# Kernel optimization log

Measured on AMD Instinct MI355X. Metric: run time of the kernel, lower is better.

## Reference

```python
import jax, jax.numpy as jnp
import numpy as np


def _cdist(a, b):
    # Euclidean pairwise distances, [N, M]
    d2 = (jnp.sum(a * a, axis=1)[:, None]
          + jnp.sum(b * b, axis=1)[None, :]
          - 2.0 * (a @ b.T))
    return jnp.sqrt(jnp.maximum(d2, 0.0))


def setup_inputs() -> dict:
    key = jax.random.key(0)
    k1, k2 = jax.random.split(key)
    N, M, D = 12288, 12288, 3
    true_pos = jax.random.normal(k1, (N, D), dtype=jnp.float32)
    pred_pos = jax.random.normal(k2, (M, D), dtype=jnp.float32)
    return {"true_pos": true_pos, "pred_pos": pred_pos}


def reference(true_pos, pred_pos):
    dists = _cdist(true_pos.astype(jnp.float32), pred_pos.astype(jnp.float32))
    mins = jnp.min(dists, axis=1)        # per true point -> nearest pred
    mins_seeds = jnp.min(dists, axis=0)  # per pred point -> nearest true
    loss = jnp.mean(mins)
    loss_seeds = jnp.mean(mins_seeds)
    just_in_case_losses = (loss, loss_seeds)
    # use_loss=True branch
    return (loss + loss_seeds, mins_seeds, just_in_case_losses)
```

## Files before the change

kernel.cpp:

```cpp
#include <hip/hip_runtime.h>
#include <hip/hip_bf16.h>
#include <cfloat>

#define BLOCK 256
#define RPT 8
#define SLICES 64

static __device__ __forceinline__ unsigned f2key(float f) {
    unsigned b = __float_as_uint(f);
    return (b & 0x80000000u) ? ~b : (b ^ 0x80000000u);
}
static __device__ __forceinline__ float key2f(unsigned k) {
    unsigned b = (k & 0x80000000u) ? (k ^ 0x80000000u) : ~k;
    return __uint_as_float(b);
}

__global__ __launch_bounds__(BLOCK) void pairmin_kernel(
    const float* __restrict__ A, const float* __restrict__ B,
    unsigned* __restrict__ min_a, unsigned* __restrict__ min_b,
    int n, int m, int colsPerSlice)
{
    const float* X; const float* Y;
    unsigned* outmin; int nx_, ny_;
    if (blockIdx.z == 0) { X = A; Y = B; outmin = min_a; nx_ = n; ny_ = m; }
    else                 { X = B; Y = A; outmin = min_b; nx_ = m; ny_ = n; }

    const int tid = threadIdx.x;
    const int rowBase = blockIdx.x * (BLOCK * RPT);
    if (rowBase >= nx_) return;

    const int colBeg = blockIdx.y * colsPerSlice;
    if (colBeg >= ny_) return;
    const int colEnd = min(colBeg + colsPerSlice, ny_);

    float nrx[RPT], nry[RPT], nrz[RPT], mn[RPT];
    bool valid[RPT];
#pragma unroll
    for (int k = 0; k < RPT; ++k) {
        int r = rowBase + tid + k * BLOCK;
        valid[k] = (r < nx_);
        int rr = valid[k] ? r : 0;
        nrx[k] = -X[3 * rr + 0];
        nry[k] = -X[3 * rr + 1];
        nrz[k] = -X[3 * rr + 2];
        mn[k] = FLT_MAX;
    }

    __shared__ float4 cols[BLOCK];
    for (int c0 = colBeg; c0 < colEnd; c0 += BLOCK) {
        const int cnt = min(BLOCK, colEnd - c0);
        if (tid < cnt) {
            const int c = c0 + tid;
            const float yx = Y[3 * c + 0];
            const float yy = Y[3 * c + 1];
            const float yz = Y[3 * c + 2];
            const float halfny = 0.5f * fmaf(yx, yx, fmaf(yy, yy, yz * yz));
            cols[tid] = make_float4(yx, yy, yz, halfny);
        }
        __syncthreads();
#pragma unroll 4
        for (int j = 0; j < cnt; ++j) {
            const float4 cc = cols[j];
#pragma unroll
            for (int k = 0; k < RPT; ++k) {
                float s = fmaf(nrx[k], cc.x,
                          fmaf(nry[k], cc.y,
                          fmaf(nrz[k], cc.z, cc.w)));
                mn[k] = fminf(mn[k], s);
            }
        }
        __syncthreads();
    }

#pragma unroll
    for (int k = 0; k < RPT; ++k) {
        if (valid[k])
            atomicMin(&outmin[rowBase + tid + k * BLOCK], f2key(mn[k]));
    }
}

#define FBLOCKS 128
__global__ __launch_bounds__(256) void finalize_kernel(
    const float* __restrict__ A, const float* __restrict__ B,
    const unsigned* __restrict__ min_a, const unsigned* __restrict__ min_b,
    float* __restrict__ hdr, float* __restrict__ out, int n, int m)
{
    const int stride = gridDim.x * 256;
    const int start = blockIdx.x * 256 + threadIdx.x;

    float sa = 0.f, sb = 0.f;
    for (int i = start; i < n; i += stride) {
        const float ax = A[3 * i + 0], ay = A[3 * i + 1], az = A[3 * i + 2];
        const float nrm = fmaf(ax, ax, fmaf(ay, ay, az * az));
        const float s  = key2f(min_a[i]);
        const float d2 = fmaxf(fmaf(2.f, s, nrm), 0.f);
        sa += sqrtf(d2);
    }
    for (int i = start; i < m; i += stride) {
        const float bx = B[3 * i + 0], by = B[3 * i + 1], bz = B[3 * i + 2];
        const float nrm = fmaf(bx, bx, fmaf(by, by, bz * bz));
        const float s  = key2f(min_b[i]);
        const float d2 = fmaxf(fmaf(2.f, s, nrm), 0.f);
        const float v = sqrtf(d2);
        out[1 + i] = v;
        sb += v;
    }

#pragma unroll
    for (int off = 32; off > 0; off >>= 1) {
        sa += __shfl_down(sa, off, 64);
        sb += __shfl_down(sb, off, 64);
    }
    __shared__ float reda[4], redb[4];
    const int wave = threadIdx.x >> 6;
    const int lane = threadIdx.x & 63;
    if (lane == 0) { reda[wave] = sa; redb[wave] = sb; }
    __syncthreads();

    if (threadIdx.x == 0) {
        float ta = reda[0] + reda[1] + reda[2] + reda[3];
        float tb = redb[0] + redb[1] + redb[2] + redb[3];
        atomicAdd(&hdr[0], ta);
        atomicAdd(&hdr[1], tb);
        __threadfence();
        unsigned ticket = atomicAdd((unsigned*)&hdr[2], 1u);
        if (ticket == (unsigned)(gridDim.x - 1)) {
            const float fa = atomicAdd(&hdr[0], 0.f);
            const float fb = atomicAdd(&hdr[1], 0.f);
            const float loss = fa / (float)n;
            const float loss_seeds = fb / (float)m;
            out[0] = loss + loss_seeds;
            out[1 + m] = loss;
            out[2 + m] = loss_seeds;
        }
    }
}

extern "C" void kernel_launch(void* const* d_in, const int* in_sizes, int n_in,
                              void* d_out, int out_size, void* d_ws, size_t ws_size,
                              hipStream_t stream) {
    const int n = in_sizes[0] / 3;
    const int m = in_sizes[1] / 3;
    const float* A = (const float*)d_in[0];
    const float* B = (const float*)d_in[1];
    float* out = (float*)d_out;

    float* hdr = (float*)d_ws;
    unsigned* min_a = (unsigned*)((char*)d_ws + 32);
    unsigned* min_b = min_a + n;

    hipMemsetAsync(d_ws, 0, 32, stream);
    hipMemsetAsync((void*)min_a, 0xFF, (size_t)(n + m) * 4, stream);

    const int maxnm = (n > m) ? n : m;
    const int gx = (maxnm + BLOCK * RPT - 1) / (BLOCK * RPT);
    const int colsPerSlice = (maxnm + SLICES - 1) / SLICES;
    dim3 grid(gx, SLICES, 2);
    pairmin_kernel<<<grid, BLOCK, 0, stream>>>(A, B, min_a, min_b, n, m, colsPerSlice);

    finalize_kernel<<<FBLOCKS, 256, 0, stream>>>(A, B, min_a, min_b, hdr, out, n, m);
}
```

Measured before the change: 90.84 us.

## Use packed FP32 FMA and per-slice partial minima instead of atomics and memsets

New measurement: 91.36 us. No clear change (+0.6%).

```diff
diff --git a/kernel.cpp b/kernel.cpp
--- a/kernel.cpp
+++ b/kernel.cpp
@@ -1,49 +1,46 @@
 #include <hip/hip_runtime.h>
-#include <hip/hip_bf16.h>
 #include <cfloat>
 
 #define BLOCK 256
 #define RPT 8
+#define PAIRS (RPT / 2)
 #define SLICES 64
 
-static __device__ __forceinline__ unsigned f2key(float f) {
-    unsigned b = __float_as_uint(f);
-    return (b & 0x80000000u) ? ~b : (b ^ 0x80000000u);
-}
-static __device__ __forceinline__ float key2f(unsigned k) {
-    unsigned b = (k & 0x80000000u) ? (k ^ 0x80000000u) : ~k;
-    return __uint_as_float(b);
-}
+typedef float v2f __attribute__((ext_vector_type(2)));
 
 __global__ __launch_bounds__(BLOCK) void pairmin_kernel(
     const float* __restrict__ A, const float* __restrict__ B,
-    unsigned* __restrict__ min_a, unsigned* __restrict__ min_b,
-    int n, int m, int colsPerSlice)
+    float* __restrict__ hdr, float* __restrict__ sbuf,
+    int n, int m, int colsPerSlice, int strideRows)
 {
-    const float* X; const float* Y;
-    unsigned* outmin; int nx_, ny_;
-    if (blockIdx.z == 0) { X = A; Y = B; outmin = min_a; nx_ = n; ny_ = m; }
-    else                 { X = B; Y = A; outmin = min_b; nx_ = m; ny_ = n; }
+    if (blockIdx.x == 0 && blockIdx.y == 0 && blockIdx.z == 0 && threadIdx.x < 8)
+        hdr[threadIdx.x] = 0.f;
+
+    const float* X; const float* Y; int nx_, ny_;
+    float* out_slice;
+    if (blockIdx.z == 0) { X = A; Y = B; nx_ = n; ny_ = m; out_slice = sbuf; }
+    else                 { X = B; Y = A; nx_ = m; ny_ = n;
+                           out_slice = sbuf + (size_t)SLICES * strideRows; }
+    out_slice += (size_t)blockIdx.y * strideRows;
 
     const int tid = threadIdx.x;
     const int rowBase = blockIdx.x * (BLOCK * RPT);
     if (rowBase >= nx_) return;
 
     const int colBeg = blockIdx.y * colsPerSlice;
-    if (colBeg >= ny_) return;
     const int colEnd = min(colBeg + colsPerSlice, ny_);
 
-    float nrx[RPT], nry[RPT], nrz[RPT], mn[RPT];
-    bool valid[RPT];
+    v2f nrx[PAIRS], nry[PAIRS], nrz[PAIRS], mn[PAIRS];
 #pragma unroll
-    for (int k = 0; k < RPT; ++k) {
-        int r = rowBase + tid + k * BLOCK;
-        valid[k] = (r < nx_);
-        int rr = valid[k] ? r : 0;
-        nrx[k] = -X[3 * rr + 0];
-        nry[k] = -X[3 * rr + 1];
-        nrz[k] = -X[3 * rr + 2];
-        mn[k] = FLT_MAX;
+    for (int p = 0; p < PAIRS; ++p) {
+        const int r0 = rowBase + tid + (2 * p) * BLOCK;
+        const int r1 = r0 + BLOCK;
+        const int rr0 = (r0 < nx_) ? r0 : 0;
+        const int rr1 = (r1 < nx_) ? r1 : 0;
+        nrx[p] = (v2f){-X[3 * rr0 + 0], -X[3 * rr1 + 0]};
+        nry[p] = (v2f){-X[3 * rr0 + 1], -X[3 * rr1 + 1]};
+        nrz[p] = (v2f){-X[3 * rr0 + 2], -X[3 * rr1 + 2]};
+        mn[p] = (v2f){FLT_MAX, FLT_MAX};
     }
 
     __shared__ float4 cols[BLOCK];
@@ -61,49 +58,53 @@
 #pragma unroll 4
         for (int j = 0; j < cnt; ++j) {
             const float4 cc = cols[j];
+            const v2f cx = cc.x, cy = cc.y, cz = cc.z, cw = cc.w;
 #pragma unroll
-            for (int k = 0; k < RPT; ++k) {
-                float s = fmaf(nrx[k], cc.x,
-                          fmaf(nry[k], cc.y,
-                          fmaf(nrz[k], cc.z, cc.w)));
-                mn[k] = fminf(mn[k], s);
+            for (int p = 0; p < PAIRS; ++p) {
+                v2f s = __builtin_elementwise_fma(nrz[p], cz, cw);
+                s = __builtin_elementwise_fma(nry[p], cy, s);
+                s = __builtin_elementwise_fma(nrx[p], cx, s);
+                mn[p] = __builtin_elementwise_min(mn[p], s);
             }
         }
         __syncthreads();
     }
 
 #pragma unroll
-    for (int k = 0; k < RPT; ++k) {
-        if (valid[k])
-            atomicMin(&outmin[rowBase + tid + k * BLOCK], f2key(mn[k]));
+    for (int p = 0; p < PAIRS; ++p) {
+        const int r0 = rowBase + tid + (2 * p) * BLOCK;
+        const int r1 = r0 + BLOCK;
+        if (r0 < nx_) out_slice[r0] = mn[p].x;
+        if (r1 < nx_) out_slice[r1] = mn[p].y;
     }
 }
 
-#define FBLOCKS 128
 __global__ __launch_bounds__(256) void finalize_kernel(
     const float* __restrict__ A, const float* __restrict__ B,
-    const unsigned* __restrict__ min_a, const unsigned* __restrict__ min_b,
-    float* __restrict__ hdr, float* __restrict__ out, int n, int m)
+    const float* __restrict__ sbuf, float* __restrict__ hdr,
+    float* __restrict__ out, int n, int m, int strideRows)
 {
-    const int stride = gridDim.x * 256;
-    const int start = blockIdx.x * 256 + threadIdx.x;
-
+    const int i = blockIdx.x * 256 + threadIdx.x;
     float sa = 0.f, sb = 0.f;
-    for (int i = start; i < n; i += stride) {
-        const float ax = A[3 * i + 0], ay = A[3 * i + 1], az = A[3 * i + 2];
+    if (i < n) {
+        float s = FLT_MAX;
+        const float* p = sbuf + i;
+#pragma unroll 8
+        for (int k = 0; k < SLICES; ++k) s = fminf(s, p[(size_t)k * strideRows]);
+        const float ax = A[3 * i], ay = A[3 * i + 1], az = A[3 * i + 2];
         const float nrm = fmaf(ax, ax, fmaf(ay, ay, az * az));
-        const float s  = key2f(min_a[i]);
-        const float d2 = fmaxf(fmaf(2.f, s, nrm), 0.f);
-        sa += sqrtf(d2);
+        sa = sqrtf(fmaxf(fmaf(2.f, s, nrm), 0.f));
     }
-    for (int i = start; i < m; i += stride) {
-        const float bx = B[3 * i + 0], by = B[3 * i + 1], bz = B[3 * i + 2];
+    if (i < m) {
+        float s = FLT_MAX;
+        const float* p = sbuf + (size_t)SLICES * strideRows + i;
+#pragma unroll 8
+        for (int k = 0; k < SLICES; ++k) s = fminf(s, p[(size_t)k * strideRows]);
+        const float bx = B[3 * i], by = B[3 * i + 1], bz = B[3 * i + 2];
         const float nrm = fmaf(bx, bx, fmaf(by, by, bz * bz));
-        const float s  = key2f(min_b[i]);
-        const float d2 = fmaxf(fmaf(2.f, s, nrm), 0.f);
-        const float v = sqrtf(d2);
+        const float v = sqrtf(fmaxf(fmaf(2.f, s, nrm), 0.f));
         out[1 + i] = v;
-        sb += v;
+        sb = v;
     }
 
 #pragma unroll
@@ -118,12 +119,12 @@
     __syncthreads();
 
     if (threadIdx.x == 0) {
-        float ta = reda[0] + reda[1] + reda[2] + reda[3];
-        float tb = redb[0] + redb[1] + redb[2] + redb[3];
+        const float ta = reda[0] + reda[1] + reda[2] + reda[3];
+        const float tb = redb[0] + redb[1] + redb[2] + redb[3];
         atomicAdd(&hdr[0], ta);
         atomicAdd(&hdr[1], tb);
         __threadfence();
-        unsigned ticket = atomicAdd((unsigned*)&hdr[2], 1u);
+        const unsigned ticket = atomicAdd((unsigned*)&hdr[2], 1u);
         if (ticket == (unsigned)(gridDim.x - 1)) {
             const float fa = atomicAdd(&hdr[0], 0.f);
             const float fb = atomicAdd(&hdr[1], 0.f);
@@ -146,17 +147,15 @@
     float* out = (float*)d_out;
 
     float* hdr = (float*)d_ws;
-    unsigned* min_a = (unsigned*)((char*)d_ws + 32);
-    unsigned* min_b = min_a + n;
-
-    hipMemsetAsync(d_ws, 0, 32, stream);
-    hipMemsetAsync((void*)min_a, 0xFF, (size_t)(n + m) * 4, stream);
+    float* sbuf = (float*)((char*)d_ws + 64);
 
     const int maxnm = (n > m) ? n : m;
     const int gx = (maxnm + BLOCK * RPT - 1) / (BLOCK * RPT);
     const int colsPerSlice = (maxnm + SLICES - 1) / SLICES;
     dim3 grid(gx, SLICES, 2);
-    pairmin_kernel<<<grid, BLOCK, 0, stream>>>(A, B, min_a, min_b, n, m, colsPerSlice);
+    pairmin_kernel<<<grid, BLOCK, 0, stream>>>(A, B, hdr, sbuf, n, m,
+                                               colsPerSlice, maxnm);
 
-    finalize_kernel<<<FBLOCKS, 256, 0, stream>>>(A, B, min_a, min_b, hdr, out, n, m);
+    const int fb = (maxnm + 255) / 256;
+    finalize_kernel<<<fb, 256, 0, stream>>>(A, B, sbuf, hdr, out, n, m, maxnm);
 }
```

## Compute squared distances with bf16 split-precision MFMA and a single shared pass

Applied to the files above, without the earlier changes.

Measured after the change: 269.8 us. +197.0%, slower.

```diff
diff --git a/kernel.cpp b/kernel.cpp
--- a/kernel.cpp
+++ b/kernel.cpp
@@ -1,10 +1,11 @@
 #include <hip/hip_runtime.h>
-#include <hip/hip_bf16.h>
 #include <cfloat>
 
-#define BLOCK 256
-#define RPT 8
-#define SLICES 64
+typedef __bf16 bf16x8 __attribute__((ext_vector_type(8)));
+typedef unsigned short ushort8 __attribute__((ext_vector_type(8)));
+typedef float f32x16 __attribute__((ext_vector_type(16)));
+
+#define S_SLICES 8
 
 static __device__ __forceinline__ unsigned f2key(float f) {
     unsigned b = __float_as_uint(f);
@@ -14,96 +15,136 @@
     unsigned b = (k & 0x80000000u) ? (k ^ 0x80000000u) : ~k;
     return __uint_as_float(b);
 }
-
-__global__ __launch_bounds__(BLOCK) void pairmin_kernel(
+static __device__ __forceinline__ unsigned short f2bf(float x) {
+    unsigned u = __float_as_uint(x);
+    return (unsigned short)((u + 0x7FFFu + ((u >> 16) & 1u)) >> 16);
+}
+static __device__ __forceinline__ float bfbits2f(unsigned short h) {
+    return __uint_as_float(((unsigned)h) << 16);
+}
+
+__global__ __launch_bounds__(256) void prep_kernel(
     const float* __restrict__ A, const float* __restrict__ B,
-    unsigned* __restrict__ min_a, unsigned* __restrict__ min_b,
-    int n, int m, int colsPerSlice)
+    ushort8* __restrict__ AF, ushort8* __restrict__ BF,
+    unsigned* __restrict__ rowkey, unsigned* __restrict__ colkey,
+    float* __restrict__ hdr, int n, int m, int RT, int CT)
 {
-    const float* X; const float* Y;
-    unsigned* outmin; int nx_, ny_;
-    if (blockIdx.z == 0) { X = A; Y = B; outmin = min_a; nx_ = n; ny_ = m; }
-    else                 { X = B; Y = A; outmin = min_b; nx_ = m; ny_ = n; }
-
-    const int tid = threadIdx.x;
-    const int rowBase = blockIdx.x * (BLOCK * RPT);
-    if (rowBase >= nx_) return;
-
-    const int colBeg = blockIdx.y * colsPerSlice;
-    if (colBeg >= ny_) return;
-    const int colEnd = min(colBeg + colsPerSlice, ny_);
-
-    float nrx[RPT], nry[RPT], nrz[RPT], mn[RPT];
-    bool valid[RPT];
-#pragma unroll
-    for (int k = 0; k < RPT; ++k) {
-        int r = rowBase + tid + k * BLOCK;
-        valid[k] = (r < nx_);
-        int rr = valid[k] ? r : 0;
-        nrx[k] = -X[3 * rr + 0];
-        nry[k] = -X[3 * rr + 1];
-        nrz[k] = -X[3 * rr + 2];
-        mn[k] = FLT_MAX;
-    }
-
-    __shared__ float4 cols[BLOCK];
-    for (int c0 = colBeg; c0 < colEnd; c0 += BLOCK) {
-        const int cnt = min(BLOCK, colEnd - c0);
-        if (tid < cnt) {
-            const int c = c0 + tid;
-            const float yx = Y[3 * c + 0];
-            const float yy = Y[3 * c + 1];
-            const float yz = Y[3 * c + 2];
-            const float halfny = 0.5f * fmaf(yx, yx, fmaf(yy, yy, yz * yz));
-            cols[tid] = make_float4(yx, yy, yz, halfny);
+    const int i = blockIdx.x * 256 + threadIdx.x;
+    if (i < 8) hdr[i] = 0.f;
+    if (i < RT * 32) rowkey[i] = 0xFFFFFFFFu;
+    if (i < CT * 32) colkey[i] = 0xFFFFFFFFu;
+    const unsigned short one = 0x3F80;
+
+    if (i < RT * 32) {
+        float x = 0.f, y = 0.f, z = 0.f, nrm = 1e30f;
+        if (i < n) { x = A[3*i]; y = A[3*i+1]; z = A[3*i+2];
+                     nrm = fmaf(x, x, fmaf(y, y, z * z)); }
+        const unsigned short hx = f2bf(x), hy = f2bf(y), hz = f2bf(z);
+        const unsigned short lx = f2bf(x - bfbits2f(hx)),
+                             ly = f2bf(y - bfbits2f(hy)),
+                             lz = f2bf(z - bfbits2f(hz));
+        const unsigned short nhx = f2bf(-2.f * bfbits2f(hx)),
+                             nhy = f2bf(-2.f * bfbits2f(hy)),
+                             nhz = f2bf(-2.f * bfbits2f(hz));
+        const unsigned short nlx = f2bf(-2.f * bfbits2f(lx)),
+                             nly = f2bf(-2.f * bfbits2f(ly)),
+                             nlz = f2bf(-2.f * bfbits2f(lz));
+        float r = nrm;
+        const unsigned short s1 = f2bf(r); r -= bfbits2f(s1);
+        const unsigned short s2 = f2bf(r); r -= bfbits2f(s2);
+        const unsigned short s3 = f2bf(r);
+        ushort8 q0 = { nhx, nhy, nhz, nhx, nhy, nhz, nlx, nly };
+        ushort8 q1 = { nlz, s1, s2, s3, one, one, one, 0 };
+        const int rt = i >> 5, l5 = i & 31;
+        AF[rt * 64 + l5]      = q0;
+        AF[rt * 64 + 32 + l5] = q1;
+    }
+    if (i < CT * 32) {
+        float x = 0.f, y = 0.f, z = 0.f, nrm = 1e30f;
+        if (i < m) { x = B[3*i]; y = B[3*i+1]; z = B[3*i+2];
+                     nrm = fmaf(x, x, fmaf(y, y, z * z)); }
+        const unsigned short hx = f2bf(x), hy = f2bf(y), hz = f2bf(z);
+        const unsigned short lx = f2bf(x - bfbits2f(hx)),
+                             ly = f2bf(y - bfbits2f(hy)),
+                             lz = f2bf(z - bfbits2f(hz));
+        float r = nrm;
+        const unsigned short s1 = f2bf(r); r -= bfbits2f(s1);
+        const unsigned short s2 = f2bf(r); r -= bfbits2f(s2);
+        const unsigned short s3 = f2bf(r);
+        ushort8 q0 = { hx, hy, hz, lx, ly, lz, hx, hy };
+        ushort8 q1 = { hz, one, one, one, s1, s2, s3, 0 };
+        const int ct = i >> 5, l5 = i & 31;
+        BF[ct * 64 + l5]      = q0;
+        BF[ct * 64 + 32 + l5] = q1;
+    }
+}
+
+__global__ __launch_bounds__(256) void pairmin_kernel(
+    const bf16x8* __restrict__ AF, const bf16x8* __restrict__ BF,
+    unsigned* __restrict__ rowkey, unsigned* __restrict__ colkey,
+    int RT, int CT)
+{
+    const int lane = threadIdx.x & 63;
+    const int wave = threadIdx.x >> 6;
+    const int rt = blockIdx.x * 4 + wave;
+    if (rt >= RT) return;
+
+    const int ctPer = (CT + S_SLICES - 1) / S_SLICES;
+    const int ctBeg = blockIdx.y * ctPer;
+    const int ctEnd = min(ctBeg + ctPer, CT);
+
+    const bf16x8 afrag = AF[rt * 64 + lane];
+
+    float macc[16];
+#pragma unroll
+    for (int r = 0; r < 16; ++r) macc[r] = FLT_MAX;
+
+    for (int ct = ctBeg; ct < ctEnd; ++ct) {
+        const bf16x8 bfrag = BF[ct * 64 + lane];
+        f32x16 C = {};
+        C = __builtin_amdgcn_mfma_f32_32x32x16_bf16(afrag, bfrag, C, 0, 0, 0);
+
+        float cm = fminf(C[0], C[1]);
+#pragma unroll
+        for (int r = 2; r < 16; ++r) cm = fminf(cm, C[r]);
+        cm = fminf(cm, __shfl_xor(cm, 32, 64));
+        atomicMin(&colkey[ct * 32 + (lane & 31)], f2key(cm));
+
+#pragma unroll
+        for (int r = 0; r < 16; ++r) macc[r] = fminf(macc[r], C[r]);
+    }
+
+#pragma unroll
+    for (int r = 0; r < 16; ++r) {
+        float v = macc[r];
+        v = fminf(v, __shfl_xor(v, 1, 64));
+        v = fminf(v, __shfl_xor(v, 2, 64));
+        v = fminf(v, __shfl_xor(v, 4, 64));
+        v = fminf(v, __shfl_xor(v, 8, 64));
+        v = fminf(v, __shfl_xor(v, 16, 64));
+        macc[r] = v;
+    }
+    if ((lane & 31) == 0) {
+        const int q4 = (lane >> 5) * 4;
+#pragma unroll
+        for (int r = 0; r < 16; ++r) {
+            const int row = (r & 3) + 8 * (r >> 2) + q4;
+            atomicMin(&rowkey[rt * 32 + row], f2key(macc[r]));
         }
-        __syncthreads();
-#pragma unroll 4
-        for (int j = 0; j < cnt; ++j) {
-            const float4 cc = cols[j];
-#pragma unroll
-            for (int k = 0; k < RPT; ++k) {
-                float s = fmaf(nrx[k], cc.x,
-                          fmaf(nry[k], cc.y,
-                          fmaf(nrz[k], cc.z, cc.w)));
-                mn[k] = fminf(mn[k], s);
-            }
-        }
-        __syncthreads();
-    }
-
-#pragma unroll
-    for (int k = 0; k < RPT; ++k) {
-        if (valid[k])
-            atomicMin(&outmin[rowBase + tid + k * BLOCK], f2key(mn[k]));
-    }
-}
-
-#define FBLOCKS 128
+    }
+}
+
 __global__ __launch_bounds__(256) void finalize_kernel(
-    const float* __restrict__ A, const float* __restrict__ B,
-    const unsigned* __restrict__ min_a, const unsigned* __restrict__ min_b,
+    const unsigned* __restrict__ rowkey, const unsigned* __restrict__ colkey,
     float* __restrict__ hdr, float* __restrict__ out, int n, int m)
 {
-    const int stride = gridDim.x * 256;
-    const int start = blockIdx.x * 256 + threadIdx.x;
-
+    const int i = blockIdx.x * 256 + threadIdx.x;
     float sa = 0.f, sb = 0.f;
-    for (int i = start; i < n; i += stride) {
-        const float ax = A[3 * i + 0], ay = A[3 * i + 1], az = A[3 * i + 2];
-        const float nrm = fmaf(ax, ax, fmaf(ay, ay, az * az));
-        const float s  = key2f(min_a[i]);
-        const float d2 = fmaxf(fmaf(2.f, s, nrm), 0.f);
-        sa += sqrtf(d2);
-    }
-    for (int i = start; i < m; i += stride) {
-        const float bx = B[3 * i + 0], by = B[3 * i + 1], bz = B[3 * i + 2];
-        const float nrm = fmaf(bx, bx, fmaf(by, by, bz * bz));
-        const float s  = key2f(min_b[i]);
-        const float d2 = fmaxf(fmaf(2.f, s, nrm), 0.f);
-        const float v = sqrtf(d2);
+    if (i < n) sa = sqrtf(fmaxf(key2f(rowkey[i]), 0.f));
+    if (i < m) {
+        const float v = sqrtf(fmaxf(key2f(colkey[i]), 0.f));
         out[1 + i] = v;
-        sb += v;
+        sb = v;
     }
 
 #pragma unroll
@@ -118,12 +159,12 @@
     __syncthreads();
 
     if (threadIdx.x == 0) {
-        float ta = reda[0] + reda[1] + reda[2] + reda[3];
-        float tb = redb[0] + redb[1] + redb[2] + redb[3];
+        const float ta = reda[0] + reda[1] + reda[2] + reda[3];
+        const float tb = redb[0] + redb[1] + redb[2] + redb[3];
         atomicAdd(&hdr[0], ta);
         atomicAdd(&hdr[1], tb);
         __threadfence();
-        unsigned ticket = atomicAdd((unsigned*)&hdr[2], 1u);
+        const unsigned ticket = atomicAdd((unsigned*)&hdr[2], 1u);
         if (ticket == (unsigned)(gridDim.x - 1)) {
             const float fa = atomicAdd(&hdr[0], 0.f);
             const float fb = atomicAdd(&hdr[1], 0.f);
@@ -145,18 +186,23 @@
     const float* B = (const float*)d_in[1];
     float* out = (float*)d_out;
 
-    float* hdr = (float*)d_ws;
-    unsigned* min_a = (unsigned*)((char*)d_ws + 32);
-    unsigned* min_b = min_a + n;
-
-    hipMemsetAsync(d_ws, 0, 32, stream);
-    hipMemsetAsync((void*)min_a, 0xFF, (size_t)(n + m) * 4, stream);
+    const int RT = (n + 31) / 32, CT = (m + 31) / 32;
+    char* p = (char*)d_ws;
+    float*    hdr    = (float*)p;     p += 64;
+    unsigned* rowkey = (unsigned*)p;  p += (size_t)RT * 32 * 4;
+    unsigned* colkey = (unsigned*)p;  p += (size_t)CT * 32 * 4;
+    ushort8*  AFw    = (ushort8*)p;   p += (size_t)RT * 64 * 16;
+    ushort8*  BFw    = (ushort8*)p;
+
+    const int maxPts = ((RT > CT) ? RT : CT) * 32;
+    prep_kernel<<<(maxPts + 255) / 256, 256, 0, stream>>>(
+        A, B, AFw, BFw, rowkey, colkey, hdr, n, m, RT, CT);
+
+    dim3 grid((RT + 3) / 4, S_SLICES);
+    pairmin_kernel<<<grid, 256, 0, stream>>>(
+        (const bf16x8*)AFw, (const bf16x8*)BFw, rowkey, colkey, RT, CT);
 
     const int maxnm = (n > m) ? n : m;
-    const int gx = (maxnm + BLOCK * RPT - 1) / (BLOCK * RPT);
-    const int colsPerSlice = (maxnm + SLICES - 1) / SLICES;
-    dim3 grid(gx, SLICES, 2);
-    pairmin_kernel<<<grid, BLOCK, 0, stream>>>(A, B, min_a, min_b, n, m, colsPerSlice);
-
-    finalize_kernel<<<FBLOCKS, 256, 0, stream>>>(A, B, min_a, min_b, hdr, out, n, m);
-}
+    finalize_kernel<<<(maxnm + 255) / 256, 256, 0, stream>>>(
+        rowkey, colkey, hdr, out, n, m);
+}
```
